# Optimization experiments

Measured on AMD Instinct MI355X. Metric: run time of the kernel, lower is better.

The kernel has to match this reference:

```python
import jax, jax.numpy as jnp
import numpy as np

VOXEL_SIZE = np.array([0.05, 0.05, 0.1], np.float32)
PC_RANGE = np.array([0.0, -40.0, -3.0, 70.4, 40.0, 1.0], np.float32)
GRID = np.round((PC_RANGE[3:] - PC_RANGE[:3]) / VOXEL_SIZE).astype(np.int64)  # (x,y,z) = (1408,1600,40)
MAX_POINTS = 35
MAX_VOXELS = 60000
N_POINTS = 2_000_000
NDIM = 4


def setup_inputs() -> dict:
    key = jax.random.key(0)
    k1, k2 = jax.random.split(key)
    span = jnp.asarray(PC_RANGE[3:] - PC_RANGE[:3])
    lo = jnp.asarray(PC_RANGE[:3])
    # uniform xyz inside the point-cloud range (slight overshoot ok; out-of-range points get dropped)
    xyz = jax.random.uniform(k1, (N_POINTS, 3), jnp.float32) * span * 1.02 + lo - 0.01 * span
    feat = jax.random.uniform(k2, (N_POINTS, NDIM - 3), jnp.float32)
    return {"points": jnp.concatenate([xyz, feat], axis=1)}


def hard_voxelize(points):
    """Faithful jit-able hard voxelization.

    Returns fixed-size (padded) outputs plus voxel_num, instead of the
    dynamically-sliced outputs of the CUDA kernel (data-dependent shapes are
    not jit-compatible). voxels[:voxel_num], coors[:voxel_num],
    num_points_per_voxel[:voxel_num] match the kernel semantics: voxels are
    numbered in order of first point appearance, points fill a voxel in
    arrival order, overflow points/voxels are dropped.
    """
    n = points.shape[0]
    gx, gy, gz = int(GRID[0]), int(GRID[1]), int(GRID[2])
    c = jnp.floor((points[:, :3] - jnp.asarray(PC_RANGE[:3])) / jnp.asarray(VOXEL_SIZE)).astype(jnp.int32)
    in_range = jnp.all((c >= 0) & (c < jnp.array([gx, gy, gz], jnp.int32)), axis=1)
    big = gx * gy * gz  # sentinel linear id for invalid points
    lin = jnp.where(in_range, (c[:, 2] * gy + c[:, 1]) * gx + c[:, 0], big)

    order = jnp.argsort(lin)  # stable: preserves arrival order within a voxel
    slin = lin[order]
    sc = c[order]
    spts = points[order]

    newg = jnp.concatenate([jnp.ones((1,), bool), slin[1:] != slin[:-1]])
    gid = jnp.cumsum(newg) - 1  # group id per sorted point (sorted-lin order)
    ar = jnp.arange(n, dtype=jnp.int32)

    grp_start = jnp.full((n,), n, jnp.int32).at[gid].min(ar)                      # sorted pos of first pt in group
    first_orig = jnp.full((n,), n, jnp.int32).at[gid].min(order.astype(jnp.int32))  # first-appearance index
    grp_valid = (jnp.zeros((n,), jnp.int32).at[gid].max((slin != big).astype(jnp.int32))) > 0

    # voxel ids assigned in order of first appearance (invalid groups pushed last)
    first_key = jnp.where(grp_valid, first_orig, n)
    perm = jnp.argsort(first_key)
    vid_of_group = jnp.zeros((n,), jnp.int32).at[perm].set(ar)

    pos = ar - grp_start[gid]          # arrival rank of point within its voxel
    vid_pt = vid_of_group[gid]
    keep = (slin != big) & (vid_pt < MAX_VOXELS) & (pos < MAX_POINTS)
    vi = jnp.where(keep, vid_pt, MAX_VOXELS)  # out-of-range -> dropped by scatter
    pi = jnp.where(keep, pos, 0)
    voxels = jnp.zeros((MAX_VOXELS, MAX_POINTS, points.shape[1]), points.dtype).at[vi, pi].set(spts, mode='drop')

    counts = jnp.zeros((n,), jnp.int32).at[gid].add((slin != big).astype(jnp.int32))
    g_ok = grp_valid & (vid_of_group < MAX_VOXELS)
    gv = jnp.where(g_ok, vid_of_group, MAX_VOXELS)
    numpv = jnp.zeros((MAX_VOXELS,), jnp.int32).at[gv].set(jnp.minimum(counts, MAX_POINTS), mode='drop')

    coors_g = sc[jnp.minimum(grp_start, n - 1)][:, ::-1]  # stored as (z, y, x) like the kernel
    coors = jnp.zeros((MAX_VOXELS, 3), jnp.int32).at[gv].set(coors_g, mode='drop')

    voxel_num = jnp.minimum(jnp.sum(grp_valid.astype(jnp.int32)), MAX_VOXELS)
    return voxels, coors, numpv, voxel_num


def reference(points):
    return hard_voxelize(points)
```

## Files before the change

kernel.cpp:

```cpp
#include <hip/hip_runtime.h>

constexpr int GX = 1408, GY = 1600, GZ = 40;
constexpr float LOX = 0.0f, LOY = -40.0f, LOZ = -3.0f;
constexpr float VSX = 0.05f, VSY = 0.05f, VSZ = 0.1f;
constexpr int MAXV = 60000, MAXP = 35;
constexpr int LINBITS = 27;
constexpr unsigned LINMASK = (1u << LINBITS) - 1;
constexpr unsigned EMPTYK = 0xFFFFFFFFu;
constexpr unsigned VINIT  = 0x7FFFFFFFu;

constexpr int NBIN   = 2048;
constexpr int LSLOT  = 2048;
constexpr int BINCAP = 1536;
constexpr int PPB    = 2048;
constexpr int HPT    = BINCAP / 256;

constexpr size_t CO_OFF = (size_t)MAXV * MAXP * 4;
constexpr size_t NP_OFF = CO_OFF + (size_t)MAXV * 3;
constexpr size_t VN_OFF = NP_OFF + (size_t)MAXV;

__device__ __forceinline__ unsigned hash22(unsigned lin) {
    return (lin * 2654435761u) >> 10;
}

__global__ __launch_bounds__(256) void k_bin(const float4* __restrict__ pts, int n,
                                             unsigned long long* __restrict__ binbuf,
                                             int* __restrict__ bincnt) {
    __shared__ int cnt[NBIN], off[NBIN], fill[NBIN];
    __shared__ int s256[256];
    __shared__ unsigned long long stage[PPB];
    __shared__ int sh_total;
    int t = threadIdx.x;
    for (int b = t; b < NBIN; b += 256) { cnt[b] = 0; fill[b] = 0; }
    __syncthreads();

    unsigned long long pair[PPB / 256];
    int bin[PPB / 256];
    int base = blockIdx.x * PPB;
    #pragma unroll
    for (int k = 0; k < PPB / 256; ++k) {
        int i = base + k * 256 + t;
        bin[k] = -1;
        if (i < n) {
            float4 p = pts[i];
            float fx = floorf((p.x - LOX) / VSX);
            float fy = floorf((p.y - LOY) / VSY);
            float fz = floorf((p.z - LOZ) / VSZ);
            if (fx >= 0.f && fy >= 0.f && fz >= 0.f &&
                fx < (float)GX && fy < (float)GY && fz < (float)GZ) {
                unsigned lin = ((unsigned)(int)fz * GY + (unsigned)(int)fy) * GX
                             + (unsigned)(int)fx;
                bin[k] = (int)(hash22(lin) >> 11);
                pair[k] = ((unsigned long long)(unsigned)i << LINBITS) | lin;
                atomicAdd(&cnt[bin[k]], 1);
            }
        }
    }
    __syncthreads();
    int b8 = t * 8, sum8 = 0;
    #pragma unroll
    for (int q = 0; q < 8; ++q) sum8 += cnt[b8 + q];
    s256[t] = sum8;
    __syncthreads();
    for (int o = 1; o < 256; o <<= 1) {
        int u = (t >= o) ? s256[t - o] : 0;
        __syncthreads();
        s256[t] += u;
        __syncthreads();
    }
    int run = s256[t] - sum8;
    #pragma unroll
    for (int q = 0; q < 8; ++q) { off[b8 + q] = run; run += cnt[b8 + q]; }
    if (t == 255) sh_total = s256[255];
    __syncthreads();
    #pragma unroll
    for (int k = 0; k < PPB / 256; ++k) {
        if (bin[k] >= 0) {
            int p = off[bin[k]] + atomicAdd(&fill[bin[k]], 1);
            stage[p] = ((unsigned long long)bin[k] << 48) | pair[k];
        }
    }
    __syncthreads();
    for (int b = t; b < NBIN; b += 256)
        if (cnt[b] > 0) fill[b] = atomicAdd(&bincnt[b], cnt[b]);
    __syncthreads();
    int total = sh_total;
    for (int j = t; j < total; j += 256) {
        unsigned long long e = stage[j];
        int b = (int)(e >> 48);
        int d = fill[b] + (j - off[b]);
        if (d < BINCAP) binbuf[(size_t)b * BINCAP + d] = e & ((1ULL << 48) - 1);
    }
}

__device__ __forceinline__ unsigned lds_insert32(unsigned* kt, unsigned* vt,
                                                 unsigned lin, unsigned idx) {
    unsigned h = hash22(lin) & (LSLOT - 1);
    while (true) {
        unsigned k = kt[h];
        if (k == EMPTYK) {
            unsigned old = atomicCAS(&kt[h], EMPTYK, lin);
            if (old == EMPTYK || old == lin) { atomicMin(&vt[h], idx); return h; }
            k = old;
        }
        if (k == lin) { atomicMin(&vt[h], idx); return h; }
        h = (h + 1) & (LSLOT - 1);
    }
}

__global__ __launch_bounds__(256) void k_flags2(const unsigned long long* __restrict__ binbuf,
                                                const int* __restrict__ bincnt,
                                                unsigned char* __restrict__ flagbyte) {
    __shared__ unsigned kt[LSLOT], vt[LSLOT];
    int t = threadIdx.x, bin = blockIdx.x;
    for (int s = t; s < LSLOT; s += 256) { kt[s] = EMPTYK; vt[s] = VINIT; }
    __syncthreads();
    int cnt = min(bincnt[bin], BINCAP);
    const unsigned long long* buf = binbuf + (size_t)bin * BINCAP;
    for (int j = t; j < cnt; j += 256) {
        unsigned long long e = buf[j];
        lds_insert32(kt, vt, (unsigned)(e & LINMASK), (unsigned)(e >> LINBITS));
    }
    __syncthreads();
    for (int s = t; s < LSLOT; s += 256)
        if (kt[s] != EMPTYK) flagbyte[vt[s]] = 1;
}

__device__ __forceinline__ unsigned nib(unsigned v) {
    return (v & 1u) | ((v >> 7) & 2u) | ((v >> 14) & 4u) | ((v >> 21) & 8u);
}

__global__ __launch_bounds__(256) void k_pack(const uint4* __restrict__ fb4,
                                              unsigned* __restrict__ flagw,
                                              int* __restrict__ wsums) {
    int gt = blockIdx.x * 256 + threadIdx.x;
    uint4 q0 = fb4[gt * 4 + 0], q1 = fb4[gt * 4 + 1];
    uint4 q2 = fb4[gt * 4 + 2], q3 = fb4[gt * 4 + 3];
    unsigned w0 = nib(q0.x) | (nib(q0.y) << 4) | (nib(q0.z) << 8)  | (nib(q0.w) << 12)
                | (nib(q1.x) << 16) | (nib(q1.y) << 20) | (nib(q1.z) << 24) | (nib(q1.w) << 28);
    unsigned w1 = nib(q2.x) | (nib(q2.y) << 4) | (nib(q2.z) << 8)  | (nib(q2.w) << 12)
                | (nib(q3.x) << 16) | (nib(q3.y) << 20) | (nib(q3.z) << 24) | (nib(q3.w) << 28);
    flagw[gt * 2]     = w0;
    flagw[gt * 2 + 1] = w1;
    int pc = __popc(w0) + __popc(w1);
    for (int o = 1; o < 64; o <<= 1) pc += __shfl_xor(pc, o);
    __shared__ int ws[4];
    int lane = threadIdx.x & 63, wid = threadIdx.x >> 6;
    if (lane == 0) ws[wid] = pc;
    __syncthreads();
    if (threadIdx.x == 0) wsums[blockIdx.x] = ws[0] + ws[1] + ws[2] + ws[3];
}

__global__ __launch_bounds__(256) void k_wscan(int* __restrict__ wsums, int nb3,
                                               float* __restrict__ vn_out) {
    __shared__ int sh[256];
    int t = threadIdx.x;
    int v = (t < nb3) ? wsums[t] : 0;
    sh[t] = v;
    __syncthreads();
    for (int o = 1; o < 256; o <<= 1) {
        int u = (t >= o) ? sh[t - o] : 0;
        __syncthreads();
        sh[t] += u;
        __syncthreads();
    }
    if (t < nb3) wsums[t] = sh[t] - v;
    if (t == 255) vn_out[0] = (float)min(sh[255], MAXV);
}

__global__ __launch_bounds__(256) void k_wbase(const unsigned* __restrict__ flagw,
                                               const int* __restrict__ wsums,
                                               int* __restrict__ wordbase) {
    int t = threadIdx.x;
    int gt = blockIdx.x * 256 + t;
    unsigned w0 = flagw[gt * 2], w1 = flagw[gt * 2 + 1];
    int p0 = __popc(w0);
    int mysum = p0 + __popc(w1);
    __shared__ int sh[256];
    sh[t] = mysum;
    __syncthreads();
    for (int o = 1; o < 256; o <<= 1) {
        int u = (t >= o) ? sh[t - o] : 0;
        __syncthreads();
        sh[t] += u;
        __syncthreads();
    }
    int excl = sh[t] - mysum + wsums[blockIdx.x];
    wordbase[gt * 2]     = excl;
    wordbase[gt * 2 + 1] = excl + p0;
}

__global__ __launch_bounds__(256) void k_fill2(const unsigned long long* __restrict__ binbuf,
                                               const int* __restrict__ bincnt,
                                               const unsigned* __restrict__ flagw,
                                               const int* __restrict__ wordbase,
                                               int* __restrict__ cursor,
                                               int* __restrict__ lists,
                                               float* __restrict__ coors_out) {
    __shared__ unsigned kt[LSLOT], vt[LSLOT];
    int t = threadIdx.x, bin = blockIdx.x;
    for (int s = t; s < LSLOT; s += 256) { kt[s] = EMPTYK; vt[s] = VINIT; }
    __syncthreads();
    int cnt = min(bincnt[bin], BINCAP);
    const unsigned long long* buf = binbuf + (size_t)bin * BINCAP;
    unsigned hmem[HPT];
    #pragma unroll
    for (int q = 0; q < HPT; ++q) {
        int j = t + q * 256;
        hmem[q] = 0;
        if (j < cnt) {
            unsigned long long e = buf[j];
            hmem[q] = lds_insert32(kt, vt, (unsigned)(e & LINMASK),
                                   (unsigned)(e >> LINBITS));
        }
    }
    __syncthreads();
    for (int s = t; s < LSLOT; s += 256) {
        unsigned k = kt[s];
        if (k == EMPTYK) continue;
        unsigned fi = vt[s];
        unsigned w = flagw[fi >> 5];
        unsigned vid = (unsigned)wordbase[fi >> 5]
                     + (unsigned)__popc(w & ((1u << (fi & 31)) - 1u));
        vt[s] = vid;
        if (vid < (unsigned)MAXV) {
            int x = (int)(k % (unsigned)GX);
            unsigned tq = k / (unsigned)GX;
            coors_out[(size_t)vid * 3 + 0] = (float)(tq / (unsigned)GY);
            coors_out[(size_t)vid * 3 + 1] = (float)(tq % (unsigned)GY);
            coors_out[(size_t)vid * 3 + 2] = (float)x;
        }
    }
    __syncthreads();
    #pragma unroll
    for (int q = 0; q < HPT; ++q) {
        int j = t + q * 256;
        if (j < cnt) {
            unsigned vid = vt[hmem[q]];
            if (vid < (unsigned)MAXV) {
                unsigned i = (unsigned)(buf[j] >> LINBITS);
                int pos = atomicAdd(&cursor[vid], 1);
                if (pos < MAXP) lists[vid * MAXP + pos] = (int)i;
            }
        }
    }
}

constexpr int VPB = 7;
__global__ __launch_bounds__(256) void k_write(const int* __restrict__ cursor,
                                               const int* __restrict__ lists,
                                               const float4* __restrict__ pts,
                                               float* __restrict__ vox_out,
                                               float* __restrict__ np_out) {
    __shared__ int sidx[VPB * MAXP];
    __shared__ int scnt[VPB];
    int t = threadIdx.x;
    int lv = t / MAXP;
    int r  = t - lv * MAXP;
    int v  = blockIdx.x * VPB + lv;
    bool act = (t < VPB * MAXP) && (v < MAXV);
    if (act && r == 0) scnt[lv] = min(cursor[v], MAXP);
    __syncthreads();
    int k = 0, myidx = 0x7fffffff;
    if (act) {
        k = scnt[lv];
        if (r < k) myidx = lists[v * MAXP + r];
        sidx[lv * MAXP + r] = myidx;
    }
    __syncthreads();
    if (!act) return;
    float4 val = make_float4(0.f, 0.f, 0.f, 0.f);
    int rank = r;
    if (r < k) {
        rank = 0;
        for (int j = 0; j < k; ++j) rank += (sidx[lv * MAXP + j] < myidx);
        val = pts[myidx];
    }
    ((float4*)vox_out)[(size_t)v * MAXP + rank] = val;
    if (r == 0) np_out[v] = (float)k;
}

extern "C" void kernel_launch(void* const* d_in, const int* in_sizes, int n_in,
                              void* d_out, int out_size, void* d_ws, size_t ws_size,
                              hipStream_t stream) {
    const float4* pts = (const float4*)d_in[0];
    int n = in_sizes[0] / 4;
    float* out = (float*)d_out;
    char* ws = (char*)d_ws;
    int nbin_blk = (n + PPB - 1) / PPB;
    int nb3 = (n + 16383) / 16384;
    size_t NBYTES_PAD = (size_t)nb3 * 16384;
    size_t NWORDS     = (size_t)nb3 * 512;

    size_t off = 0;
    unsigned char* flagbyte = (unsigned char*)(ws + off);
    off += NBYTES_PAD;
    int* cursor = (int*)(ws + off);
    off += (size_t)MAXV * 4;
    int* bincnt = (int*)(ws + off);
    off += (size_t)NBIN * 4;
    size_t zero_bytes = off;
    off = (off + 255) & ~(size_t)255;
    unsigned long long* binbuf = (unsigned long long*)(ws + off);
    off += (size_t)NBIN * BINCAP * 8;
    unsigned* flagw = (unsigned*)(ws + off);
    off += NWORDS * 4;
    int* wordbase = (int*)(ws + off);
    off += NWORDS * 4;
    int* wsums = (int*)(ws + off);
    off += 1024;
    int* lists = (int*)(ws + off);

    hipMemsetAsync(flagbyte, 0, zero_bytes, stream);
    hipMemsetAsync(out + CO_OFF, 0, (size_t)(out_size - (int)CO_OFF) * 4, stream);

    k_bin   <<<nbin_blk, 256, 0, stream>>>(pts, n, binbuf, bincnt);
    k_flags2<<<NBIN, 256, 0, stream>>>(binbuf, bincnt, flagbyte);
    k_pack  <<<nb3, 256, 0, stream>>>((const uint4*)flagbyte, flagw, wsums);
    k_wscan <<<1, 256, 0, stream>>>(wsums, nb3, out + VN_OFF);
    k_wbase <<<nb3, 256, 0, stream>>>(flagw, wsums, wordbase);
    k_fill2 <<<NBIN, 256, 0, stream>>>(binbuf, bincnt, flagw, wordbase,
                                       cursor, lists, out + CO_OFF);
    k_write <<<(MAXV + VPB - 1) / VPB, 256, 0, stream>>>(cursor, lists, pts,
                                                         out, out + NP_OFF);
}
```

Measured before the change: 201.3 us.

## Simplify binning scatter and fuse block-sum scan into word-base kernel

The binning kernel drops its shared-memory prefix scan and staging buffer. Each point now keeps its local rank from the shared atomic and writes straight to its global bin slot after one global atomic per bin. Points per block double, which halves the number of blocks and global atomics. The separate single-block scan kernel is folded into k_wbase, where every block redundantly rescans the block sums, removing one launch. The cost is uncoalesced scattered global writes in place of the staged, bin-grouped writes.

```diff
diff --git a/kernel.cpp b/kernel.cpp
--- a/kernel.cpp
+++ b/kernel.cpp
@@ -12,7 +12,8 @@
 constexpr int NBIN   = 2048;
 constexpr int LSLOT  = 2048;
 constexpr int BINCAP = 1536;
-constexpr int PPB    = 2048;
+constexpr int PPB    = 4096;
+constexpr int RND    = PPB / 256;
 constexpr int HPT    = BINCAP / 256;
 
 constexpr size_t CO_OFF = (size_t)MAXV * MAXP * 4;
@@ -26,21 +27,18 @@
 __global__ __launch_bounds__(256) void k_bin(const float4* __restrict__ pts, int n,
                                              unsigned long long* __restrict__ binbuf,
                                              int* __restrict__ bincnt) {
-    __shared__ int cnt[NBIN], off[NBIN], fill[NBIN];
-    __shared__ int s256[256];
-    __shared__ unsigned long long stage[PPB];
-    __shared__ int sh_total;
+    __shared__ int cnt[NBIN], gbase[NBIN];
     int t = threadIdx.x;
-    for (int b = t; b < NBIN; b += 256) { cnt[b] = 0; fill[b] = 0; }
-    __syncthreads();
-
-    unsigned long long pair[PPB / 256];
-    int bin[PPB / 256];
+    for (int b = t; b < NBIN; b += 256) cnt[b] = 0;
+    __syncthreads();
+
+    unsigned lin[RND];
+    unsigned rb[RND];
     int base = blockIdx.x * PPB;
     #pragma unroll
-    for (int k = 0; k < PPB / 256; ++k) {
+    for (int k = 0; k < RND; ++k) {
         int i = base + k * 256 + t;
-        bin[k] = -1;
+        rb[k] = 0xFFFFFFFFu;
         if (i < n) {
             float4 p = pts[i];
             float fx = floorf((p.x - LOX) / VSX);
@@ -48,48 +46,29 @@
             float fz = floorf((p.z - LOZ) / VSZ);
             if (fx >= 0.f && fy >= 0.f && fz >= 0.f &&
                 fx < (float)GX && fy < (float)GY && fz < (float)GZ) {
-                unsigned lin = ((unsigned)(int)fz * GY + (unsigned)(int)fy) * GX
-                             + (unsigned)(int)fx;
-                bin[k] = (int)(hash22(lin) >> 11);
-                pair[k] = ((unsigned long long)(unsigned)i << LINBITS) | lin;
-                atomicAdd(&cnt[bin[k]], 1);
+                unsigned lv = ((unsigned)(int)fz * GY + (unsigned)(int)fy) * GX
+                            + (unsigned)(int)fx;
+                unsigned b = hash22(lv) >> 11;
+                unsigned r = (unsigned)atomicAdd(&cnt[b], 1);
+                rb[k] = (b << 16) | r;
+                lin[k] = lv;
             }
         }
     }
     __syncthreads();
-    int b8 = t * 8, sum8 = 0;
+    for (int b = t; b < NBIN; b += 256)
+        if (cnt[b] > 0) gbase[b] = atomicAdd(&bincnt[b], cnt[b]);
+    __syncthreads();
     #pragma unroll
-    for (int q = 0; q < 8; ++q) sum8 += cnt[b8 + q];
-    s256[t] = sum8;
-    __syncthreads();
-    for (int o = 1; o < 256; o <<= 1) {
-        int u = (t >= o) ? s256[t - o] : 0;
-        __syncthreads();
-        s256[t] += u;
-        __syncthreads();
-    }
-    int run = s256[t] - sum8;
-    #pragma unroll
-    for (int q = 0; q < 8; ++q) { off[b8 + q] = run; run += cnt[b8 + q]; }
-    if (t == 255) sh_total = s256[255];
-    __syncthreads();
-    #pragma unroll
-    for (int k = 0; k < PPB / 256; ++k) {
-        if (bin[k] >= 0) {
-            int p = off[bin[k]] + atomicAdd(&fill[bin[k]], 1);
-            stage[p] = ((unsigned long long)bin[k] << 48) | pair[k];
-        }
-    }
-    __syncthreads();
-    for (int b = t; b < NBIN; b += 256)
-        if (cnt[b] > 0) fill[b] = atomicAdd(&bincnt[b], cnt[b]);
-    __syncthreads();
-    int total = sh_total;
-    for (int j = t; j < total; j += 256) {
-        unsigned long long e = stage[j];
-        int b = (int)(e >> 48);
-        int d = fill[b] + (j - off[b]);
-        if (d < BINCAP) binbuf[(size_t)b * BINCAP + d] = e & ((1ULL << 48) - 1);
+    for (int k = 0; k < RND; ++k) {
+        if (rb[k] != 0xFFFFFFFFu) {
+            unsigned b = rb[k] >> 16;
+            int d = gbase[b] + (int)(rb[k] & 0xFFFFu);
+            unsigned i = (unsigned)(base + k * 256 + t);
+            if (d < BINCAP)
+                binbuf[(size_t)b * BINCAP + d] =
+                    ((unsigned long long)i << LINBITS) | lin[k];
+        }
     }
 }
 
@@ -151,8 +130,10 @@
     if (threadIdx.x == 0) wsums[blockIdx.x] = ws[0] + ws[1] + ws[2] + ws[3];
 }
 
-__global__ __launch_bounds__(256) void k_wscan(int* __restrict__ wsums, int nb3,
-                                               float* __restrict__ vn_out) {
+__global__ __launch_bounds__(256) void k_wbase(const unsigned* __restrict__ flagw,
+                                               const int* __restrict__ wsums,
+                                               int* __restrict__ wordbase,
+                                               int nb3, float* __restrict__ vn_out) {
     __shared__ int sh[256];
     int t = threadIdx.x;
     int v = (t < nb3) ? wsums[t] : 0;
@@ -164,19 +145,14 @@
         sh[t] += u;
         __syncthreads();
     }
-    if (t < nb3) wsums[t] = sh[t] - v;
-    if (t == 255) vn_out[0] = (float)min(sh[255], MAXV);
-}
-
-__global__ __launch_bounds__(256) void k_wbase(const unsigned* __restrict__ flagw,
-                                               const int* __restrict__ wsums,
-                                               int* __restrict__ wordbase) {
-    int t = threadIdx.x;
+    int blkbase = (blockIdx.x == 0) ? 0 : sh[blockIdx.x - 1];
+    if (blockIdx.x == 0 && t == 0)
+        vn_out[0] = (float)min(sh[nb3 - 1], MAXV);
+    __syncthreads();
     int gt = blockIdx.x * 256 + t;
     unsigned w0 = flagw[gt * 2], w1 = flagw[gt * 2 + 1];
     int p0 = __popc(w0);
     int mysum = p0 + __popc(w1);
-    __shared__ int sh[256];
     sh[t] = mysum;
     __syncthreads();
     for (int o = 1; o < 256; o <<= 1) {
@@ -185,7 +161,7 @@
         sh[t] += u;
         __syncthreads();
     }
-    int excl = sh[t] - mysum + wsums[blockIdx.x];
+    int excl = sh[t] - mysum + blkbase;
     wordbase[gt * 2]     = excl;
     wordbase[gt * 2 + 1] = excl + p0;
 }
@@ -317,8 +293,7 @@
     k_bin   <<<nbin_blk, 256, 0, stream>>>(pts, n, binbuf, bincnt);
     k_flags2<<<NBIN, 256, 0, stream>>>(binbuf, bincnt, flagbyte);
     k_pack  <<<nb3, 256, 0, stream>>>((const uint4*)flagbyte, flagw, wsums);
-    k_wscan <<<1, 256, 0, stream>>>(wsums, nb3, out + VN_OFF);
-    k_wbase <<<nb3, 256, 0, stream>>>(flagw, wsums, wordbase);
+    k_wbase <<<nb3, 256, 0, stream>>>(flagw, wsums, wordbase, nb3, out + VN_OFF);
     k_fill2 <<<NBIN, 256, 0, stream>>>(binbuf, bincnt, flagw, wordbase,
                                        cursor, lists, out + CO_OFF);
     k_write <<<(MAXV + VPB - 1) / VPB, 256, 0, stream>>>(cursor, lists, pts,
```

Result: faster. 182.3 us (-9.4%).
